# Optimization experiments

Hardware: AMD Instinct MI355X
Metric: run time of the kernel (lower is better)

Reference implementation:

```python
import jax, jax.numpy as jnp
import numpy as np

# ---- module hyperparameters (match BlurredNoise defaults) ----
CHANNELS = 1024
BLUR_WIDTHS = 128
NOISE_CHANNELS = CHANNELS // BLUR_WIDTHS  # 8
MIN_SR = 250.0
MAX_SR = 10000.0
CUTOFF = 2.0
WIDTH = 12.0
SR_BASE = 2.0
NORM_PER_FILTER = 1.0
KERNEL_SIZE = int(np.ceil(MAX_SR / 2))  # 5000

BATCH = 2
SEQ_LENGTH = 4096
IN_SEQ = SEQ_LENGTH + KERNEL_SIZE - 1  # 9095


def _kaiser_beta(a):
    # scipy.signal.kaiser_beta
    if a > 50:
        return 0.1102 * (a - 8.7)
    if a > 21:
        return 0.5842 * (a - 21) ** 0.4 + 0.07886 * (a - 21)
    return 0.0


def _firwin_lowpass(numtaps, cutoff, width, fs):
    # Re-implementation of scipy.signal.firwin(numtaps, cutoff, width=width, fs=fs)
    # (lowpass, pass_zero=True, Kaiser window chosen from transition width).
    nyq = 0.5 * fs
    atten = 2.285 * (numtaps - 1) * np.pi * (width / nyq) + 7.95  # kaiser_atten
    beta = _kaiser_beta(atten)
    win = np.kaiser(numtaps, beta)
    m = np.arange(numtaps) - (numtaps - 1) / 2.0
    right = cutoff / nyq
    h = right * np.sinc(right * m)  # ideal lowpass impulse response
    h = h * win
    h = h / h.sum()  # normalize DC gain to 1 (scale at f=0, pass_zero)
    return h.astype(np.float32)


def _build_filters():
    log_min = np.log(MIN_SR) / np.log(SR_BASE)
    log_max = np.log(MAX_SR) / np.log(SR_BASE)
    sampling_rates = SR_BASE ** np.linspace(log_min, log_max, BLUR_WIDTHS)
    sampling_rates = np.clip(sampling_rates, MIN_SR, MAX_SR)
    blur_filters = np.zeros((BLUR_WIDTHS, KERNEL_SIZE), dtype=np.float32)
    for i, sr in enumerate(sampling_rates):
        num_taps = int(np.ceil(sr / 2))
        blur_filters[i, -num_taps:] = _firwin_lowpass(num_taps, CUTOFF, WIDTH, sr)
    output_scale = 1.0 / np.sqrt((blur_filters ** 2).sum(axis=1))  # (128,)
    output_scale = output_scale.reshape(1, BLUR_WIDTHS, 1).astype(np.float32)
    return blur_filters, output_scale


def setup_inputs() -> dict:
    key = jax.random.key(0)
    noise = jax.random.normal(key, (BATCH, NOISE_CHANNELS, IN_SEQ), dtype=jnp.float32)
    bf, os_ = _build_filters()
    return {
        "noise": noise,
        "blur_filters": jnp.asarray(bf),
        "output_scale": jnp.asarray(os_),
    }


def reference(noise, blur_filters, output_scale):
    # noise: (n, c, t_in) with c = NOISE_CHANNELS
    n, c, t = noise.shape
    # einops.repeat 'n c t -> (n c) b t' followed by grouped conv (groups=b)
    # with per-group single input channel is exactly a standard conv with
    # 1 input channel and b output channels.
    x = noise.reshape(n * c, 1, t)                       # (n*c, 1, t_in)
    k = blur_filters[:, None, :]                         # (b, 1, K) OIW
    feats = jax.lax.conv_general_dilated(
        x, k, window_strides=(1,), padding="VALID",
        dimension_numbers=("NCH", "OIH", "NCH"))          # (n*c, b, T)
    feats = feats * (1.0 + NORM_PER_FILTER * (output_scale - 1.0))
    T = feats.shape[-1]
    # '(n c) b t -> n (c b) t'
    return feats.reshape(n, c * BLUR_WIDTHS, T)
```

## Files before the change

kernel.cpp:

```cpp
#include <hip/hip_runtime.h>
#include <hip/hip_bf16.h>


#define KS      5000
#define IN_SEQ  9095
#define T_OUT   4096
#define NBC     16
#define NF      128
#define NSTEP   313
#define SWZSTEP 328
#define CSTRIDE 1056
#define XBUF    (8*CSTRIDE)
#define XPS     9344
#define XTAIL   256
#define SWZ_BYTES (4*SWZSTEP*1024)

typedef __attribute__((ext_vector_type(8)))  short v8s;
typedef __attribute__((ext_vector_type(4)))  float v4f;
typedef __attribute__((ext_vector_type(16))) float v16f;

__device__ __forceinline__ unsigned short f2b(float v) {
  union { __hip_bfloat16 h; unsigned short u; } cv;
  cv.h = __float2bfloat16(v);
  return cv.u;
}

__global__ void build_pre(const float* __restrict__ filt,
                          const float* __restrict__ noise,
                          unsigned short* __restrict__ swz,
                          float* __restrict__ xpad) {
  const int b = blockIdx.x;
  if (b < 313) {
    const int i = b * 256 + threadIdx.x;
    if (i >= 4 * NSTEP * 64) return;
    const int lane = i & 63;
    const int frag = i >> 6;
    const int ft = frag / NSTEP;
    const int s  = frag - ft * NSTEP;
    const int col = lane & 31;
    const int hi  = lane >> 5;
    const int jg0 = KS - 16 * (s + 1) + 8 * hi;
    const float* row = filt + (size_t)(ft * 32 + col) * KS;
    unsigned short o[8];
    #pragma unroll
    for (int j = 0; j < 8; ++j) {
      int jg = jg0 + j;
      int jc = jg < 0 ? 0 : jg;
      float v = (jg >= 0) ? row[jc] : 0.0f;
      o[j] = f2b(v);
    }
    *(uint4*)(swz + (((size_t)(ft * SWZSTEP + s)) << 9) + (lane << 3)) = *(uint4*)o;
  } else {
    const int i = (b - 313) * 256 + threadIdx.x;
    if (i >= NBC * XPS + XTAIL) return;
    const int r = i / XPS;
    const int pcol = i - r * XPS;
    const int lg = pcol - 32;
    xpad[i] = (r < NBC && lg >= 0 && lg < IN_SEQ) ? noise[r * IN_SEQ + lg] : 0.0f;
  }
}

template<int W, int U, int SB, int D>
__device__ __forceinline__ void run_seg(
    const char* __restrict__ swzg, const float* __restrict__ xn,
    char* xb, int xrd_off, int t0, int lane, v16f (&acc)[4])
{
  v8s breg[D][W];
  v8s areg[2];
  const char* xrd = xb + xrd_off;

  const char* sp[W];
  #pragma unroll
  for (int w = 0; w < W; ++w)
    sp[w] = swzg + (((size_t)((4 - W + w) * SWZSTEP + SB)) << 10) + 16 * lane;

  {
    const int wb = t0 + KS - 16 * (SB + U);
    float4 xr[4];
    #pragma unroll
    for (int ii = 0; ii < 4; ++ii)
      xr[ii] = *(const float4*)(xn + (wb + 8 * lane + 4 * ii));
    const float* f = (const float*)xr;
    unsigned u8v[8];
    #pragma unroll
    for (int j = 0; j < 8; ++j)
      u8v[j] = (unsigned)f2b(f[2 * j]) | ((unsigned)f2b(f[2 * j + 1]) << 16);
    auto AL = [](unsigned hi, unsigned lo) { return (lo >> 16) | (hi << 16); };
    char* buf = xb + 16 * lane;
    #pragma unroll
    for (int c = 0; c < 8; ++c) {
      const int h = c >> 1;
      uint4 wv;
      if ((c & 1) == 0)
        wv = (uint4){u8v[h], u8v[h + 1], u8v[h + 2], u8v[h + 3]};
      else
        wv = (uint4){AL(u8v[h + 1], u8v[h]),     AL(u8v[h + 2], u8v[h + 1]),
                     AL(u8v[h + 3], u8v[h + 2]), AL(u8v[h + 4], u8v[h + 3])};
      *(uint4*)(buf + c * CSTRIDE) = wv;
    }
  }

  #pragma unroll
  for (int d = 0; d < D; ++d)
    #pragma unroll
    for (int w = 0; w < W; ++w)
      breg[d][w] = *(const v8s*)(sp[w] + (d << 10));
  areg[0] = *(const v8s*)(xrd + 32 * (U - 1));

  #pragma unroll
  for (int i = 0; i < U; ++i) {
    const int ap = i & 1;
    const int un = (i + 1 < U) ? (U - 2 - i) : (U - 1);
    areg[ap ^ 1] = *(const v8s*)(xrd + 32 * un);
    #pragma unroll
    for (int w = 0; w < W; ++w)
      acc[4 - W + w] = __builtin_amdgcn_mfma_f32_32x32x16_bf16(
          areg[ap], breg[i % D][w], acc[4 - W + w], 0, 0, 0);
    #pragma unroll
    for (int w = 0; w < W; ++w)
      breg[i % D][w] = *(const v8s*)(sp[w] + ((i + D) << 10));
  }
}

__global__ __launch_bounds__(64, 2) void blur_mfma(
    const float* __restrict__ xpad,
    const unsigned short* __restrict__ swz,
    const float* __restrict__ scale,
    float* __restrict__ out)
{
  __shared__ __align__(16) char xb[XBUF];
  const int lane = threadIdx.x;
  const int b  = blockIdx.x;
  const int bc = b >> 7;
  const int t0 = (b & 127) << 5;
  const int row = lane & 31, hi = lane >> 5;
  const float* __restrict__ xn = xpad + (size_t)bc * XPS + 32;
  const char* swzg = (const char*)swz;
  const int xrd_off = (row & 7) * CSTRIDE + 16 * (row >> 3) + 16 * hi;

  v16f acc[4];
  #pragma unroll
  for (int n = 0; n < 4; ++n)
    #pragma unroll
    for (int j = 0; j < 16; ++j) acc[n][j] = 0.0f;

  run_seg<4, 20,   0,  3>(swzg, xn, xb, xrd_off, t0, lane, acc);
  run_seg<3, 29,  20,  4>(swzg, xn, xb, xrd_off, t0, lane, acc);
  run_seg<2, 25,  49,  6>(swzg, xn, xb, xrd_off, t0, lane, acc);
  run_seg<2, 25,  74,  6>(swzg, xn, xb, xrd_off, t0, lane, acc);
  run_seg<2, 25,  99,  6>(swzg, xn, xb, xrd_off, t0, lane, acc);
  run_seg<1, 27, 124, 12>(swzg, xn, xb, xrd_off, t0, lane, acc);
  run_seg<1, 27, 151, 12>(swzg, xn, xb, xrd_off, t0, lane, acc);
  run_seg<1, 27, 178, 12>(swzg, xn, xb, xrd_off, t0, lane, acc);
  run_seg<1, 27, 205, 12>(swzg, xn, xb, xrd_off, t0, lane, acc);
  run_seg<1, 27, 232, 12>(swzg, xn, xb, xrd_off, t0, lane, acc);
  run_seg<1, 27, 259, 12>(swzg, xn, xb, xrd_off, t0, lane, acc);
  run_seg<1, 27, 286, 12>(swzg, xn, xb, xrd_off, t0, lane, acc);

  #pragma unroll
  for (int n = 0; n < 4; ++n) {
    const int F = 32 * n + row;
    const float sc = scale[F];
    float* op = out + (size_t)(bc * NF + F) * T_OUT + t0 + 4 * hi;
    #pragma unroll
    for (int r2 = 0; r2 < 4; ++r2) {
      v4f o = {acc[n][4 * r2] * sc, acc[n][4 * r2 + 1] * sc,
               acc[n][4 * r2 + 2] * sc, acc[n][4 * r2 + 3] * sc};
      *(v4f*)(op + 8 * r2) = o;
    }
  }
}

extern "C" void kernel_launch(void* const* d_in, const int* in_sizes, int n_in,
                              void* d_out, int out_size, void* d_ws, size_t ws_size,
                              hipStream_t stream) {
  const float* noise = (const float*)d_in[0];
  const float* filt  = (const float*)d_in[1];
  const float* scale = (const float*)d_in[2];
  float* out = (float*)d_out;

  unsigned short* swz = (unsigned short*)d_ws;
  float* xpad = (float*)((char*)d_ws + SWZ_BYTES);

  const int pad_blocks = (NBC * XPS + XTAIL + 255) / 256;
  build_pre<<<313 + pad_blocks, 256, 0, stream>>>(filt, noise, swz, xpad);
  blur_mfma<<<2048, 64, 0, stream>>>(xpad, swz, scale, out);
}
```

Before: 122.1 us.

## Compute two 32-step output tiles per block to reuse filter fragments

Each block now covers 64 output time steps instead of 32, holding two sets of MFMA accumulators. Every filter fragment loaded into registers feeds two MFMAs, one per time tile, which halves global filter traffic per output. The A-operand prefetch is widened to two tiles, and the first two segment lengths are rebalanced so the staged input window still fits the shared buffer. The cost is twice the accumulator registers, launch bounds lowered to one block, and half as many blocks in the grid, which reduces occupancy and latency hiding.

```diff
diff --git a/kernel.cpp b/kernel.cpp
--- a/kernel.cpp
+++ b/kernel.cpp
@@ -63,10 +63,10 @@
 template<int W, int U, int SB, int D>
 __device__ __forceinline__ void run_seg(
     const char* __restrict__ swzg, const float* __restrict__ xn,
-    char* xb, int xrd_off, int t0, int lane, v16f (&acc)[4])
+    char* xb, int xrd_off, int t0, int lane, v16f (&acc)[2][4])
 {
   v8s breg[D][W];
-  v8s areg[2];
+  v8s areg[4][2];
   const char* xrd = xb + xrd_off;
 
   const char* sp[W];
@@ -105,24 +105,31 @@
     #pragma unroll
     for (int w = 0; w < W; ++w)
       breg[d][w] = *(const v8s*)(sp[w] + (d << 10));
-  areg[0] = *(const v8s*)(xrd + 32 * (U - 1));
+  #pragma unroll
+  for (int j = 0; j < 2; ++j)
+    #pragma unroll
+    for (int m = 0; m < 2; ++m)
+      areg[j][m] = *(const v8s*)(xrd + 64 * m + 32 * (U - 1 - j));
 
   #pragma unroll
   for (int i = 0; i < U; ++i) {
-    const int ap = i & 1;
-    const int un = (i + 1 < U) ? (U - 2 - i) : (U - 1);
-    areg[ap ^ 1] = *(const v8s*)(xrd + 32 * un);
+    const int un = (i + 2 < U) ? (U - 3 - i) : 0;
+    #pragma unroll
+    for (int m = 0; m < 2; ++m)
+      areg[(i + 2) & 3][m] = *(const v8s*)(xrd + 64 * m + 32 * un);
     #pragma unroll
     for (int w = 0; w < W; ++w)
-      acc[4 - W + w] = __builtin_amdgcn_mfma_f32_32x32x16_bf16(
-          areg[ap], breg[i % D][w], acc[4 - W + w], 0, 0, 0);
+      #pragma unroll
+      for (int m = 0; m < 2; ++m)
+        acc[m][4 - W + w] = __builtin_amdgcn_mfma_f32_32x32x16_bf16(
+            areg[i & 3][m], breg[i % D][w], acc[m][4 - W + w], 0, 0, 0);
     #pragma unroll
     for (int w = 0; w < W; ++w)
       breg[i % D][w] = *(const v8s*)(sp[w] + ((i + D) << 10));
   }
 }
 
-__global__ __launch_bounds__(64, 2) void blur_mfma(
+__global__ __launch_bounds__(64, 1) void blur_mfma(
     const float* __restrict__ xpad,
     const unsigned short* __restrict__ swz,
     const float* __restrict__ scale,
@@ -131,21 +138,23 @@
   __shared__ __align__(16) char xb[XBUF];
   const int lane = threadIdx.x;
   const int b  = blockIdx.x;
-  const int bc = b >> 7;
-  const int t0 = (b & 127) << 5;
+  const int bc = b >> 6;
+  const int t0 = (b & 63) << 6;
   const int row = lane & 31, hi = lane >> 5;
   const float* __restrict__ xn = xpad + (size_t)bc * XPS + 32;
   const char* swzg = (const char*)swz;
   const int xrd_off = (row & 7) * CSTRIDE + 16 * (row >> 3) + 16 * hi;
 
-  v16f acc[4];
+  v16f acc[2][4];
   #pragma unroll
-  for (int n = 0; n < 4; ++n)
+  for (int m = 0; m < 2; ++m)
     #pragma unroll
-    for (int j = 0; j < 16; ++j) acc[n][j] = 0.0f;
+    for (int n = 0; n < 4; ++n)
+      #pragma unroll
+      for (int j = 0; j < 16; ++j) acc[m][n][j] = 0.0f;
 
-  run_seg<4, 20,   0,  3>(swzg, xn, xb, xrd_off, t0, lane, acc);
-  run_seg<3, 29,  20,  4>(swzg, xn, xb, xrd_off, t0, lane, acc);
+  run_seg<4, 21,   0,  3>(swzg, xn, xb, xrd_off, t0, lane, acc);
+  run_seg<3, 28,  21,  4>(swzg, xn, xb, xrd_off, t0, lane, acc);
   run_seg<2, 25,  49,  6>(swzg, xn, xb, xrd_off, t0, lane, acc);
   run_seg<2, 25,  74,  6>(swzg, xn, xb, xrd_off, t0, lane, acc);
   run_seg<2, 25,  99,  6>(swzg, xn, xb, xrd_off, t0, lane, acc);
@@ -158,17 +167,19 @@
   run_seg<1, 27, 286, 12>(swzg, xn, xb, xrd_off, t0, lane, acc);
 
   #pragma unroll
-  for (int n = 0; n < 4; ++n) {
-    const int F = 32 * n + row;
-    const float sc = scale[F];
-    float* op = out + (size_t)(bc * NF + F) * T_OUT + t0 + 4 * hi;
+  for (int m = 0; m < 2; ++m)
     #pragma unroll
-    for (int r2 = 0; r2 < 4; ++r2) {
-      v4f o = {acc[n][4 * r2] * sc, acc[n][4 * r2 + 1] * sc,
-               acc[n][4 * r2 + 2] * sc, acc[n][4 * r2 + 3] * sc};
-      *(v4f*)(op + 8 * r2) = o;
+    for (int n = 0; n < 4; ++n) {
+      const int F = 32 * n + row;
+      const float sc = scale[F];
+      float* op = out + (size_t)(bc * NF + F) * T_OUT + t0 + 32 * m + 4 * hi;
+      #pragma unroll
+      for (int r2 = 0; r2 < 4; ++r2) {
+        v4f o = {acc[m][n][4 * r2] * sc, acc[m][n][4 * r2 + 1] * sc,
+                 acc[m][n][4 * r2 + 2] * sc, acc[m][n][4 * r2 + 3] * sc};
+        *(v4f*)(op + 8 * r2) = o;
+      }
     }
-  }
 }
 
 extern "C" void kernel_launch(void* const* d_in, const int* in_sizes, int n_in,
@@ -184,5 +195,5 @@
 
   const int pad_blocks = (NBC * XPS + XTAIL + 255) / 256;
   build_pre<<<313 + pad_blocks, 256, 0, stream>>>(filt, noise, swz, xpad);
-  blur_mfma<<<2048, 64, 0, stream>>>(xpad, swz, scale, out);
+  blur_mfma<<<1024, 64, 0, stream>>>(xpad, swz, scale, out);
 }
```

New measurement: 144.4 us. 18.3% more time.
